# Kernel optimization log

Hardware: AMD Instinct MI355X
Metric: run time of the kernel (lower is better)

Reference implementation:

```python
import jax, jax.numpy as jnp
import numpy as np

WS = 15  # window_size


def setup_inputs() -> dict:
    key = jax.random.key(0)
    k1, k2, k3, k4 = jax.random.split(key, 4)
    x = jax.random.normal(k1, (4, 256, 200, 200), dtype=jnp.float32)
    theta_w = jax.random.normal(k2, (144, 256), dtype=jnp.float32) * 0.01
    phi_w = jax.random.normal(k3, (144, 256), dtype=jnp.float32) * 0.01
    # zero_init=False: use a small random projection so the output is nontrivial
    proj_w = jax.random.normal(k4, (256, 256), dtype=jnp.float32) * 0.01
    return {"x": x, "theta_w": theta_w, "phi_w": phi_w, "proj_w": proj_w}


def reference(x, theta_w, phi_w, proj_w):
    B, C, H, W = x.shape
    ws = WS
    pad_h = (ws - H % ws) % ws
    pad_w = (ws - W % ws) % ws
    xp = jnp.pad(x, ((0, 0), (0, 0), (0, pad_h), (0, pad_w)), mode='reflect')
    Hp, Wp = xp.shape[2], xp.shape[3]
    Nh, Nw = Hp // ws, Wp // ws
    # extract non-overlapping ws x ws windows -> (B*Nh*Nw, C, ws*ws)
    xw = (xp.reshape(B, C, Nh, ws, Nw, ws)
            .transpose(0, 2, 4, 1, 3, 5)
            .reshape(B * Nh * Nw, C, ws * ws))
    Ce = theta_w.shape[0]  # 144
    theta = jnp.einsum('ec,bcn->bne', theta_w, xw)   # (Bp, N, Ce)
    phi = jnp.einsum('ec,bcm->bem', phi_w, xw)       # (Bp, Ce, N)
    aff = jnp.einsum('bne,bem->bnm', theta, phi) / jnp.sqrt(jnp.asarray(Ce, x.dtype))
    aff = jax.nn.softmax(aff, axis=-1)               # (Bp, N, N)
    out = jnp.einsum('bnm,bcm->bcn', aff, xw)        # attention-weighted g (= x windows)
    out = jnp.einsum('oc,bcn->bon', proj_w, out)     # 1x1 projection
    # fold windows back -> (B, C, Hp, Wp), crop, residual
    y = (out.reshape(B, Nh, Nw, C, ws, ws)
            .transpose(0, 3, 1, 4, 2, 5)
            .reshape(B, C, Hp, Wp))
    y = y[:, :, :H, :W]
    return x + y
```

## Files before the change

kernel.cpp:

```cpp
#include <hip/hip_runtime.h>


#define WS_   15
#define B_    4
#define C_    256
#define H_    200
#define H2    (H_*H_)
#define NHW   14
#define NWIN  (B_*NHW*NHW)
#define NPOS  225
#define NWAVE 16

#define PT_STRIDE 144
#define Z_STRIDE  232
#define TT_STRIDE 144
#define ST_STRIDE 240
#define TT_SLOT   (16*TT_STRIDE)
#define ST_SLOT   (16*ST_STRIDE)

#define XT_OFF    0
#define PT_OFF    57600
#define Z_OFF     90144
#define TT_OFF    149536
#define ST_OFF    154144
#define GS_OFF    161824
#define LDS_BYTES 162016

typedef __attribute__((ext_vector_type(4))) float floatx4;

__device__ inline int pack4(float a, float b, float c, float d) {
    int pk = __builtin_amdgcn_cvt_pk_fp8_f32(a, b, 0, false);
    return __builtin_amdgcn_cvt_pk_fp8_f32(c, d, pk, true);
}
__device__ inline long wfrag8(const float* p, float scale) {
    floatx4 a = *(const floatx4*)p;
    floatx4 b = *(const floatx4*)(p + 4);
    int lo = 0, hi = 0;
    lo = __builtin_amdgcn_cvt_pk_fp8_f32(a[0]*scale, a[1]*scale, lo, false);
    lo = __builtin_amdgcn_cvt_pk_fp8_f32(a[2]*scale, a[3]*scale, lo, true);
    hi = __builtin_amdgcn_cvt_pk_fp8_f32(b[0]*scale, b[1]*scale, hi, false);
    hi = __builtin_amdgcn_cvt_pk_fp8_f32(b[2]*scale, b[3]*scale, hi, true);
    return ((long)(unsigned)lo) | (((long)(unsigned)hi) << 32);
}
__device__ inline long ldsfrag(const char* p) { return *(const long*)p; }

#define MFMA8(a,b,c) __builtin_amdgcn_mfma_f32_16x16x32_fp8_fp8((a),(b),(c),0,0,0)

__device__ inline void bar_lds() {
    asm volatile("s_waitcnt lgkmcnt(0)" ::: "memory");
    __builtin_amdgcn_s_barrier();
}

__global__ __launch_bounds__(1024) void wnl_kernel(
    const float* __restrict__ x, const float* __restrict__ theta_w,
    const float* __restrict__ phi_w, const float* __restrict__ proj_w,
    float* __restrict__ out)
{
    __shared__ char lds[LDS_BYTES];
    char*  XT    = lds + XT_OFF;
    char*  PT    = lds + PT_OFF;
    char*  Zs    = lds + Z_OFF;
    char*  TT    = lds + TT_OFF;
    char*  ST    = lds + ST_OFF;
    float* gsumf = (float*)(lds + GS_OFF);

    const int tid  = threadIdx.x;
    const int wv   = tid >> 6;
    const int lane = tid & 63;
    const int q    = lane >> 4;
    const int l16  = lane & 15;
    const int swl  = (l16 & 7) << 3;

    const int wid  = blockIdx.x;
    const int b    = wid / (NHW*NHW);
    const int rr   = wid % (NHW*NHW);
    const int row0 = (rr / NHW) * WS_;
    const int col0 = (rr % NHW) * WS_;
    const float* xb = x + (size_t)b * C_ * H2;

    long thw[8], wA[8], wB[8];
    if (wv < 9) {
        const float* wrow = theta_w + (wv*16 + l16) * C_ + q*8;
        #pragma unroll
        for (int ck = 0; ck < 8; ++ck) thw[ck] = wfrag8(wrow + ck*32, 16.f);
    }
    {
        const float* wrowA = (wv < 9)
            ? (phi_w  + (wv*16     + l16) * C_ + q*8)
            : (proj_w + ((wv-9)*16 + l16) * C_ + q*8);
        #pragma unroll
        for (int ck = 0; ck < 8; ++ck) wA[ck] = wfrag8(wrowA + ck*32, 16.f);
        if (wv < 9) {
            const float* wrowB = proj_w + ((wv+7)*16 + l16) * C_ + q*8;
            #pragma unroll
            for (int ck = 0; ck < 8; ++ck) wB[ck] = wfrag8(wrowB + ck*32, 16.f);
        }
    }

    if (tid < 48) gsumf[tid] = 0.f;

    {
        const int gn  = tid & 255;
        const int gc0 = (tid >> 8) << 2;
        if (gn < NPOS) {
            int wr = row0 + gn / WS_;
            int wc = col0 + gn % WS_;
            int gr = (wr < H_) ? wr : (2*H_ - 2 - wr);
            int gc = (wc < H_) ? wc : (2*H_ - 2 - wc);
            const float* p = xb + (size_t)gc0 * H2 + (gr * H_ + gc);
            char* dst = XT + gn * 256;
            const int sw = (gn & 7) << 3;
            float a0 = p[0], a1 = p[H2], a2 = p[2*(size_t)H2], a3 = p[3*(size_t)H2];
            for (int k = 0; k < 16; ++k) {
                float b0=0.f, b1=0.f, b2=0.f, b3=0.f;
                if (k < 15) {
                    const float* pn = p + (size_t)(16*(k+1)) * H2;
                    b0 = pn[0]; b1 = pn[H2]; b2 = pn[2*(size_t)H2]; b3 = pn[3*(size_t)H2];
                }
                *(int*)(dst + ((gc0 + 16*k) ^ sw)) = pack4(a0, a1, a2, a3);
                a0=b0; a1=b1; a2=b2; a3=b3;
            }
        }
    }
    bar_lds();

    if (wv < 9) {
        for (int mt = 0; mt < 15; ++mt) {
            long xf[8];
            const char* xbase = XT + (mt*16 + l16) * 256;
            #pragma unroll
            for (int ck = 0; ck < 8; ++ck)
                xf[ck] = ldsfrag(xbase + ((q*8 + ck*32) ^ swl));
            floatx4 accP = {0.f,0.f,0.f,0.f};
            floatx4 accZ = {0.f,0.f,0.f,0.f};
            #pragma unroll
            for (int ck = 0; ck < 8; ++ck) {
                accP = MFMA8(wA[ck], xf[ck], accP);
                accZ = MFMA8(xf[ck], wB[ck], accZ);
            }
            if (mt*16 + l16 < NPOS)
                *(int*)(PT + (mt*16 + l16) * PT_STRIDE + wv*16 + 4*q) =
                    pack4(accP[0], accP[1], accP[2], accP[3]);
            {
                float z[4];
                #pragma unroll
                for (int r = 0; r < 4; ++r) {
                    int m = mt*16 + 4*q + r;
                    z[r] = (m < NPOS) ? accZ[r] : 0.f;
                }
                if (mt*16 + 4*q < Z_STRIDE)
                    *(int*)(Zs + ((wv+7)*16 + l16) * Z_STRIDE + mt*16 + 4*q) =
                        pack4(z[0], z[1], z[2], z[3]);
            }
            if (mt == 0) {
                floatx4 accT = {0.f,0.f,0.f,0.f};
                #pragma unroll
                for (int ck = 0; ck < 8; ++ck)
                    accT = MFMA8(thw[ck], xf[ck], accT);
                *(int*)(TT + l16 * TT_STRIDE + wv*16 + 4*q) =
                    pack4(accT[0], accT[1], accT[2], accT[3]);
            }
        }
    } else {
        const int ot = wv - 9;
        for (int mt = 0; mt < 15; ++mt) {
            long xf[8];
            const char* xbase = XT + (mt*16 + l16) * 256;
            #pragma unroll
            for (int ck = 0; ck < 8; ++ck)
                xf[ck] = ldsfrag(xbase + ((q*8 + ck*32) ^ swl));
            floatx4 accZ = {0.f,0.f,0.f,0.f};
            #pragma unroll
            for (int ck = 0; ck < 8; ++ck)
                accZ = MFMA8(xf[ck], wA[ck], accZ);
            float z[4];
            #pragma unroll
            for (int r = 0; r < 4; ++r) {
                int m = mt*16 + 4*q + r;
                z[r] = (m < NPOS) ? accZ[r] : 0.f;
            }
            if (mt*16 + 4*q < Z_STRIDE)
                *(int*)(Zs + (ot*16 + l16) * Z_STRIDE + mt*16 + 4*q) =
                    pack4(z[0], z[1], z[2], z[3]);
        }
    }
    bar_lds();

    long pfr[5];
    if (wv < 15) {
        const char* prow = PT + (wv*16 + l16) * PT_STRIDE + q*8;
        #pragma unroll
        for (int kk = 0; kk < 4; ++kk) pfr[kk] = ldsfrag(prow + kk*32);
        pfr[4] = (q < 2) ? ldsfrag(PT + (wv*16 + l16)*PT_STRIDE + 128 + q*8) : 0L;
    }
    long zfr[8];
    {
        const char* zrow = Zs + (wv*16 + l16) * Z_STRIDE + q*8;
        #pragma unroll
        for (int km = 0; km < 7; ++km) zfr[km] = ldsfrag(zrow + km*32);
        zfr[7] = (q == 0) ? ldsfrag(Zs + (wv*16 + l16)*Z_STRIDE + 224) : 0L;
    }

    for (int nt = 0; nt <= 15; ++nt) {
        const bool do_aff = (nt < 15) && (wv < 15);
        const bool do_pv  = (nt >= 1);
        const bool do_tt  = (nt < 14) && (wv < 9);

        float xr0=0.f, xr1=0.f, xr2=0.f, xr3=0.f;
        size_t gbase = 0; bool valid = false;
        if (do_pv) {
            const int n_o  = (nt-1)*16 + l16;
            const int wr_o = row0 + n_o / WS_;
            const int wc_o = col0 + n_o % WS_;
            valid = (n_o < NPOS) && (wr_o < H_) && (wc_o < H_);
            gbase = (((size_t)b * C_ + (wv*16 + q*4)) * H_ + wr_o) * H_ + wc_o;
            if (valid) {
                xr0 = x[gbase];
                xr1 = x[gbase + H2];
                xr2 = x[gbase + 2*(size_t)H2];
                xr3 = x[gbase + 3*(size_t)H2];
            }
        }

        floatx4 aacc = {0.f,0.f,0.f,0.f};
        if (do_aff) {
            const char* trow = TT + (nt & 1) * TT_SLOT + l16 * TT_STRIDE + q*8;
            long tfr[5];
            #pragma unroll
            for (int kk = 0; kk < 4; ++kk) tfr[kk] = ldsfrag(trow + kk*32);
            tfr[4] = (q < 2)
                ? ldsfrag(TT + (nt & 1) * TT_SLOT + l16 * TT_STRIDE + 128 + q*8) : 0L;
            #pragma unroll
            for (int kk = 0; kk < 4; ++kk)
                aacc = MFMA8(pfr[kk], tfr[kk], aacc);
            aacc = MFMA8(pfr[4], tfr[4], aacc);
        }
        float pe[4] = {0.f,0.f,0.f,0.f};
        if (do_aff) {
            #pragma unroll
            for (int r = 0; r < 4; ++r) {
                int m = wv*16 + 4*q + r;
                pe[r] = (m < NPOS) ? __expf(aacc[r] * (1.0f/3072.0f)) : 0.f;
            }
        }

        long sfr[8];
        if (do_pv) {
            const char* srow = ST + ((nt-1) & 1) * ST_SLOT + l16 * ST_STRIDE + q*8;
            #pragma unroll
            for (int km = 0; km < 7; ++km) sfr[km] = ldsfrag(srow + km*32);
            sfr[7] = (q == 0)
                ? ldsfrag(ST + ((nt-1) & 1) * ST_SLOT + l16 * ST_STRIDE + 224) : 0L;
        }
        long xf[8];
        if (do_tt) {
            const char* xbase = XT + ((nt+1)*16 + l16) * 256;
            #pragma unroll
            for (int ck = 0; ck < 8; ++ck)
                xf[ck] = ldsfrag(xbase + ((q*8 + ck*32) ^ swl));
        }

        if (do_aff) {
            *(int*)(ST + (nt & 1) * ST_SLOT + l16 * ST_STRIDE + wv*16 + 4*q) =
                pack4(pe[0], pe[1], pe[2], pe[3]);
            float s = pe[0] + pe[1] + pe[2] + pe[3];
            s += __shfl_xor(s, 16);
            s += __shfl_xor(s, 32);
            if (lane < 16) atomicAdd(&gsumf[(nt % 3)*16 + lane], s);
        }
        if (do_tt) {
            floatx4 tacc = {0.f,0.f,0.f,0.f};
            #pragma unroll
            for (int ck = 0; ck < 8; ++ck)
                tacc = MFMA8(thw[ck], xf[ck], tacc);
            *(int*)(TT + ((nt+1) & 1) * TT_SLOT + l16 * TT_STRIDE + wv*16 + 4*q) =
                pack4(tacc[0], tacc[1], tacc[2], tacc[3]);
        }
        if (do_pv) {
            floatx4 acc = {0.f,0.f,0.f,0.f};
            #pragma unroll
            for (int km = 0; km < 7; ++km)
                acc = MFMA8(zfr[km], sfr[km], acc);
            acc = MFMA8(zfr[7], sfr[7], acc);
            float gs   = gsumf[((nt-1) % 3)*16 + l16];
            float sinv = __builtin_amdgcn_rcpf(16.0f * gs);
            if (valid) {
                __builtin_nontemporal_store(xr0 + acc[0]*sinv, &out[gbase]);
                __builtin_nontemporal_store(xr1 + acc[1]*sinv, &out[gbase + H2]);
                __builtin_nontemporal_store(xr2 + acc[2]*sinv, &out[gbase + 2*(size_t)H2]);
                __builtin_nontemporal_store(xr3 + acc[3]*sinv, &out[gbase + 3*(size_t)H2]);
            }
        }
        if (wv == 15 && lane < 16 && nt < 15)
            gsumf[((nt+1) % 3)*16 + lane] = 0.f;

        if (nt < 15) bar_lds();
    }
}

extern "C" void kernel_launch(void* const* d_in, const int* in_sizes, int n_in,
                              void* d_out, int out_size, void* d_ws, size_t ws_size,
                              hipStream_t stream) {
    (void)in_sizes; (void)n_in; (void)out_size; (void)d_ws; (void)ws_size;
    const float* x   = (const float*)d_in[0];
    const float* tw  = (const float*)d_in[1];
    const float* pw  = (const float*)d_in[2];
    const float* prw = (const float*)d_in[3];
    wnl_kernel<<<NWIN, 1024, 0, stream>>>(x, tw, pw, prw, (float*)d_out);
}
```

Before: 623.2 us.

## Restructure window kernel so each wave owns one query tile end-to-end

```diff
diff --git a/kernel.cpp b/kernel.cpp
--- a/kernel.cpp
+++ b/kernel.cpp
@@ -11,20 +11,19 @@
 #define NPOS  225
 #define NWAVE 16
 
+#define XT_STRIDE 264
 #define PT_STRIDE 144
-#define Z_STRIDE  232
-#define TT_STRIDE 144
-#define ST_STRIDE 240
-#define TT_SLOT   (16*TT_STRIDE)
-#define ST_SLOT   (16*ST_STRIDE)
-
-#define XT_OFF    0
-#define PT_OFF    57600
-#define Z_OFF     90144
-#define TT_OFF    149536
-#define ST_OFF    154144
-#define GS_OFF    161824
-#define LDS_BYTES 162016
+#define Z_STRIDE  240
+
+#define XT_OFF 0
+#define PT_OFF 59400
+#define Z_OFF  91800
+#define LDS_BYTES 153240
+
+#define THQ_OFF 0
+#define PHQ_OFF 36864
+#define PRQ_OFF 73728
+#define WQ_BYTES 139264
 
 typedef __attribute__((ext_vector_type(4))) float floatx4;
 
@@ -32,17 +31,8 @@
     int pk = __builtin_amdgcn_cvt_pk_fp8_f32(a, b, 0, false);
     return __builtin_amdgcn_cvt_pk_fp8_f32(c, d, pk, true);
 }
-__device__ inline long wfrag8(const float* p, float scale) {
-    floatx4 a = *(const floatx4*)p;
-    floatx4 b = *(const floatx4*)(p + 4);
-    int lo = 0, hi = 0;
-    lo = __builtin_amdgcn_cvt_pk_fp8_f32(a[0]*scale, a[1]*scale, lo, false);
-    lo = __builtin_amdgcn_cvt_pk_fp8_f32(a[2]*scale, a[3]*scale, lo, true);
-    hi = __builtin_amdgcn_cvt_pk_fp8_f32(b[0]*scale, b[1]*scale, hi, false);
-    hi = __builtin_amdgcn_cvt_pk_fp8_f32(b[2]*scale, b[3]*scale, hi, true);
-    return ((long)(unsigned)lo) | (((long)(unsigned)hi) << 32);
-}
 __device__ inline long ldsfrag(const char* p) { return *(const long*)p; }
+__device__ inline long gfrag(const unsigned char* p) { return *(const long*)p; }
 
 #define MFMA8(a,b,c) __builtin_amdgcn_mfma_f32_16x16x32_fp8_fp8((a),(b),(c),0,0,0)
 
@@ -51,25 +41,38 @@
     __builtin_amdgcn_s_barrier();
 }
 
+__global__ void prep_kernel(const float* __restrict__ tw,
+                            const float* __restrict__ pw,
+                            const float* __restrict__ prw,
+                            unsigned char* __restrict__ wq)
+{
+    int idx = blockIdx.x * blockDim.x + threadIdx.x;
+    for (int d = idx; d < WQ_BYTES / 4; d += gridDim.x * blockDim.x) {
+        int base = d * 4;
+        const float* src;
+        int off;
+        if (base < PHQ_OFF)      { src = tw;  off = base; }
+        else if (base < PRQ_OFF) { src = pw;  off = base - PHQ_OFF; }
+        else                     { src = prw; off = base - PRQ_OFF; }
+        const float* p = src + off;
+        ((int*)wq)[d] = pack4(p[0]*16.f, p[1]*16.f, p[2]*16.f, p[3]*16.f);
+    }
+}
+
 __global__ __launch_bounds__(1024) void wnl_kernel(
-    const float* __restrict__ x, const float* __restrict__ theta_w,
-    const float* __restrict__ phi_w, const float* __restrict__ proj_w,
+    const float* __restrict__ x, const unsigned char* __restrict__ wq,
     float* __restrict__ out)
 {
     __shared__ char lds[LDS_BYTES];
-    char*  XT    = lds + XT_OFF;
-    char*  PT    = lds + PT_OFF;
-    char*  Zs    = lds + Z_OFF;
-    char*  TT    = lds + TT_OFF;
-    char*  ST    = lds + ST_OFF;
-    float* gsumf = (float*)(lds + GS_OFF);
+    char* XT = lds + XT_OFF;
+    char* PT = lds + PT_OFF;
+    char* Zs = lds + Z_OFF;
 
     const int tid  = threadIdx.x;
     const int wv   = tid >> 6;
     const int lane = tid & 63;
     const int q    = lane >> 4;
     const int l16  = lane & 15;
-    const int swl  = (l16 & 7) << 3;
 
     const int wid  = blockIdx.x;
     const int b    = wid / (NHW*NHW);
@@ -78,26 +81,21 @@
     const int col0 = (rr % NHW) * WS_;
     const float* xb = x + (size_t)b * C_ * H2;
 
-    long thw[8], wA[8], wB[8];
+    const unsigned char* thetaq = wq + THQ_OFF;
+    const unsigned char* phiq   = wq + PHQ_OFF;
+    const unsigned char* projq  = wq + PRQ_OFF;
+
+    long wAf[8], wBf[8];
     if (wv < 9) {
-        const float* wrow = theta_w + (wv*16 + l16) * C_ + q*8;
-        #pragma unroll
-        for (int ck = 0; ck < 8; ++ck) thw[ck] = wfrag8(wrow + ck*32, 16.f);
-    }
-    {
-        const float* wrowA = (wv < 9)
-            ? (phi_w  + (wv*16     + l16) * C_ + q*8)
-            : (proj_w + ((wv-9)*16 + l16) * C_ + q*8);
-        #pragma unroll
-        for (int ck = 0; ck < 8; ++ck) wA[ck] = wfrag8(wrowA + ck*32, 16.f);
-        if (wv < 9) {
-            const float* wrowB = proj_w + ((wv+7)*16 + l16) * C_ + q*8;
-            #pragma unroll
-            for (int ck = 0; ck < 8; ++ck) wB[ck] = wfrag8(wrowB + ck*32, 16.f);
-        }
-    }
-
-    if (tid < 48) gsumf[tid] = 0.f;
+        const unsigned char* pa = phiq + (wv*16 + l16)*256 + q*8;
+        const unsigned char* pb = projq + ((wv+7)*16 + l16)*256 + q*8;
+        #pragma unroll
+        for (int ck = 0; ck < 8; ++ck) { wAf[ck] = gfrag(pa + ck*32); wBf[ck] = gfrag(pb + ck*32); }
+    } else {
+        const unsigned char* pa = projq + ((wv-9)*16 + l16)*256 + q*8;
+        #pragma unroll
+        for (int ck = 0; ck < 8; ++ck) wAf[ck] = gfrag(pa + ck*32);
+    }
 
     {
         const int gn  = tid & 255;
@@ -108,8 +106,7 @@
             int gr = (wr < H_) ? wr : (2*H_ - 2 - wr);
             int gc = (wc < H_) ? wc : (2*H_ - 2 - wc);
             const float* p = xb + (size_t)gc0 * H2 + (gr * H_ + gc);
-            char* dst = XT + gn * 256;
-            const int sw = (gn & 7) << 3;
+            char* dst = XT + gn * XT_STRIDE;
             float a0 = p[0], a1 = p[H2], a2 = p[2*(size_t)H2], a3 = p[3*(size_t)H2];
             for (int k = 0; k < 16; ++k) {
                 float b0=0.f, b1=0.f, b2=0.f, b3=0.f;
@@ -117,7 +114,7 @@
                     const float* pn = p + (size_t)(16*(k+1)) * H2;
                     b0 = pn[0]; b1 = pn[H2]; b2 = pn[2*(size_t)H2]; b3 = pn[3*(size_t)H2];
                 }
-                *(int*)(dst + ((gc0 + 16*k) ^ sw)) = pack4(a0, a1, a2, a3);
+                *(int*)(dst + gc0 + 16*k) = pack4(a0, a1, a2, a3);
                 a0=b0; a1=b1; a2=b2; a3=b3;
             }
         }
@@ -127,184 +124,179 @@
     if (wv < 9) {
         for (int mt = 0; mt < 15; ++mt) {
             long xf[8];
-            const char* xbase = XT + (mt*16 + l16) * 256;
-            #pragma unroll
-            for (int ck = 0; ck < 8; ++ck)
-                xf[ck] = ldsfrag(xbase + ((q*8 + ck*32) ^ swl));
+            const char* xrow = XT + (mt*16 + l16) * XT_STRIDE + q*8;
+            #pragma unroll
+            for (int ck = 0; ck < 8; ++ck) xf[ck] = ldsfrag(xrow + ck*32);
             floatx4 accP = {0.f,0.f,0.f,0.f};
             floatx4 accZ = {0.f,0.f,0.f,0.f};
             #pragma unroll
             for (int ck = 0; ck < 8; ++ck) {
-                accP = MFMA8(wA[ck], xf[ck], accP);
-                accZ = MFMA8(xf[ck], wB[ck], accZ);
+                accP = MFMA8(wAf[ck], xf[ck], accP);
+                accZ = MFMA8(xf[ck], wBf[ck], accZ);
             }
             if (mt*16 + l16 < NPOS)
                 *(int*)(PT + (mt*16 + l16) * PT_STRIDE + wv*16 + 4*q) =
                     pack4(accP[0], accP[1], accP[2], accP[3]);
-            {
-                float z[4];
-                #pragma unroll
-                for (int r = 0; r < 4; ++r) {
-                    int m = mt*16 + 4*q + r;
-                    z[r] = (m < NPOS) ? accZ[r] : 0.f;
-                }
-                if (mt*16 + 4*q < Z_STRIDE)
-                    *(int*)(Zs + ((wv+7)*16 + l16) * Z_STRIDE + mt*16 + 4*q) =
-                        pack4(z[0], z[1], z[2], z[3]);
-            }
-            if (mt == 0) {
-                floatx4 accT = {0.f,0.f,0.f,0.f};
-                #pragma unroll
-                for (int ck = 0; ck < 8; ++ck)
-                    accT = MFMA8(thw[ck], xf[ck], accT);
-                *(int*)(TT + l16 * TT_STRIDE + wv*16 + 4*q) =
-                    pack4(accT[0], accT[1], accT[2], accT[3]);
-            }
+            float z[4];
+            #pragma unroll
+            for (int r = 0; r < 4; ++r) {
+                int m = mt*16 + 4*q + r;
+                z[r] = (m < NPOS) ? accZ[r] : 0.f;
+            }
+            *(int*)(Zs + ((wv+7)*16 + l16) * Z_STRIDE + mt*16 + 4*q) =
+                pack4(z[0], z[1], z[2], z[3]);
         }
     } else {
         const int ot = wv - 9;
         for (int mt = 0; mt < 15; ++mt) {
             long xf[8];
-            const char* xbase = XT + (mt*16 + l16) * 256;
+            const char* xrow = XT + (mt*16 + l16) * XT_STRIDE + q*8;
+            #pragma unroll
+            for (int ck = 0; ck < 8; ++ck) xf[ck] = ldsfrag(xrow + ck*32);
+            floatx4 accZ = {0.f,0.f,0.f,0.f};
             #pragma unroll
             for (int ck = 0; ck < 8; ++ck)
-                xf[ck] = ldsfrag(xbase + ((q*8 + ck*32) ^ swl));
-            floatx4 accZ = {0.f,0.f,0.f,0.f};
-            #pragma unroll
-            for (int ck = 0; ck < 8; ++ck)
-                accZ = MFMA8(xf[ck], wA[ck], accZ);
+                accZ = MFMA8(xf[ck], wAf[ck], accZ);
             float z[4];
             #pragma unroll
             for (int r = 0; r < 4; ++r) {
                 int m = mt*16 + 4*q + r;
                 z[r] = (m < NPOS) ? accZ[r] : 0.f;
             }
-            if (mt*16 + 4*q < Z_STRIDE)
-                *(int*)(Zs + (ot*16 + l16) * Z_STRIDE + mt*16 + 4*q) =
-                    pack4(z[0], z[1], z[2], z[3]);
+            *(int*)(Zs + (ot*16 + l16) * Z_STRIDE + mt*16 + 4*q) =
+                pack4(z[0], z[1], z[2], z[3]);
         }
     }
     bar_lds();
 
-    long pfr[5];
     if (wv < 15) {
-        const char* prow = PT + (wv*16 + l16) * PT_STRIDE + q*8;
-        #pragma unroll
-        for (int kk = 0; kk < 4; ++kk) pfr[kk] = ldsfrag(prow + kk*32);
-        pfr[4] = (q < 2) ? ldsfrag(PT + (wv*16 + l16)*PT_STRIDE + 128 + q*8) : 0L;
-    }
-    long zfr[8];
-    {
-        const char* zrow = Zs + (wv*16 + l16) * Z_STRIDE + q*8;
-        #pragma unroll
-        for (int km = 0; km < 7; ++km) zfr[km] = ldsfrag(zrow + km*32);
-        zfr[7] = (q == 0) ? ldsfrag(Zs + (wv*16 + l16)*Z_STRIDE + 224) : 0L;
-    }
-
-    for (int nt = 0; nt <= 15; ++nt) {
-        const bool do_aff = (nt < 15) && (wv < 15);
-        const bool do_pv  = (nt >= 1);
-        const bool do_tt  = (nt < 14) && (wv < 9);
-
+        const int nt = wv;
+        const int srcA = l16 + ((q & 1) << 5);
+        const int srcB = srcA + 16;
+
+        long xf[8];
+        {
+            const char* xrow = XT + (nt*16 + l16) * XT_STRIDE + q*8;
+            #pragma unroll
+            for (int ck = 0; ck < 8; ++ck) xf[ck] = ldsfrag(xrow + ck*32);
+        }
+
+        int pkT[9];
+        #pragma unroll
+        for (int et = 0; et < 9; ++et) {
+            const unsigned char* tp = thetaq + (et*16 + l16)*256 + q*8;
+            long tf[8];
+            #pragma unroll
+            for (int ck = 0; ck < 8; ++ck) tf[ck] = gfrag(tp + ck*32);
+            floatx4 acc = {0.f,0.f,0.f,0.f};
+            #pragma unroll
+            for (int ck = 0; ck < 8; ++ck)
+                acc = MFMA8(tf[ck], xf[ck], acc);
+            pkT[et] = pack4(acc[0], acc[1], acc[2], acc[3]);
+        }
+        long tfr[5];
+        #pragma unroll
+        for (int kk = 0; kk < 4; ++kk) {
+            int a0 = __shfl(pkT[2*kk],   srcA);
+            int a1 = __shfl(pkT[2*kk+1], srcA);
+            int b0 = __shfl(pkT[2*kk],   srcB);
+            int b1 = __shfl(pkT[2*kk+1], srcB);
+            unsigned lo = (q >= 2) ? (unsigned)a1 : (unsigned)a0;
+            unsigned hi = (q >= 2) ? (unsigned)b1 : (unsigned)b0;
+            tfr[kk] = (long)lo | ((long)hi << 32);
+        }
+        {
+            int a8 = __shfl(pkT[8], srcA);
+            int b8 = __shfl(pkT[8], srcB);
+            tfr[4] = (q < 2) ? ((long)(unsigned)a8 | ((long)(unsigned)b8 << 32)) : 0L;
+        }
+
+        float ssum = 0.f;
+        int pm[15];
+        #pragma unroll
+        for (int mt = 0; mt < 15; ++mt) {
+            const char* prow = PT + (mt*16 + l16) * PT_STRIDE + q*8;
+            floatx4 aacc = {0.f,0.f,0.f,0.f};
+            #pragma unroll
+            for (int kk = 0; kk < 4; ++kk)
+                aacc = MFMA8(ldsfrag(prow + kk*32), tfr[kk], aacc);
+            long p4 = (q < 2) ? ldsfrag(PT + (mt*16 + l16)*PT_STRIDE + 128 + q*8) : 0L;
+            aacc = MFMA8(p4, tfr[4], aacc);
+            float pe[4];
+            #pragma unroll
+            for (int r = 0; r < 4; ++r) {
+                int m = mt*16 + 4*q + r;
+                pe[r] = (m < NPOS) ? __expf(aacc[r] * (1.0f/3072.0f)) : 0.f;
+                ssum += pe[r];
+            }
+            pm[mt] = pack4(pe[0], pe[1], pe[2], pe[3]);
+        }
+        ssum += __shfl_xor(ssum, 16);
+        ssum += __shfl_xor(ssum, 32);
+        const float sinv = __builtin_amdgcn_rcpf(16.0f * ssum);
+
+        long sfr[8];
+        #pragma unroll
+        for (int km = 0; km < 7; ++km) {
+            int a0 = __shfl(pm[2*km],   srcA);
+            int a1 = __shfl(pm[2*km+1], srcA);
+            int b0 = __shfl(pm[2*km],   srcB);
+            int b1 = __shfl(pm[2*km+1], srcB);
+            unsigned lo = (q >= 2) ? (unsigned)a1 : (unsigned)a0;
+            unsigned hi = (q >= 2) ? (unsigned)b1 : (unsigned)b0;
+            sfr[km] = (long)lo | ((long)hi << 32);
+        }
+        {
+            int a8 = __shfl(pm[14], srcA);
+            int b8 = __shfl(pm[14], srcB);
+            sfr[7] = (q == 0) ? ((long)(unsigned)a8 | ((long)(unsigned)b8 << 32)) : 0L;
+        }
+
+        const int n_o  = nt*16 + l16;
+        const int wr_o = row0 + n_o / WS_;
+        const int wc_o = col0 + n_o % WS_;
+        const bool valid = (n_o < NPOS) && (wr_o < H_) && (wc_o < H_);
+        const size_t gb0 = (size_t)b * C_ * H2 + ((size_t)wr_o * H_ + wc_o);
         float xr0=0.f, xr1=0.f, xr2=0.f, xr3=0.f;
-        size_t gbase = 0; bool valid = false;
-        if (do_pv) {
-            const int n_o  = (nt-1)*16 + l16;
-            const int wr_o = row0 + n_o / WS_;
-            const int wc_o = col0 + n_o % WS_;
-            valid = (n_o < NPOS) && (wr_o < H_) && (wc_o < H_);
-            gbase = (((size_t)b * C_ + (wv*16 + q*4)) * H_ + wr_o) * H_ + wc_o;
+        if (valid) {
+            const float* p = x + gb0 + (size_t)(4*q) * H2;
+            xr0 = p[0]; xr1 = p[H2]; xr2 = p[2*(size_t)H2]; xr3 = p[3*(size_t)H2];
+        }
+        #pragma unroll
+        for (int ot = 0; ot < 16; ++ot) {
+            float nx0=0.f, nx1=0.f, nx2=0.f, nx3=0.f;
+            if (ot < 15 && valid) {
+                const float* p = x + gb0 + (size_t)((ot+1)*16 + 4*q) * H2;
+                nx0 = p[0]; nx1 = p[H2]; nx2 = p[2*(size_t)H2]; nx3 = p[3*(size_t)H2];
+            }
+            const char* zrow = Zs + (ot*16 + l16) * Z_STRIDE + q*8;
+            floatx4 acc = {0.f,0.f,0.f,0.f};
+            #pragma unroll
+            for (int km = 0; km < 7; ++km)
+                acc = MFMA8(ldsfrag(zrow + km*32), sfr[km], acc);
+            long z7 = (q < 2) ? ldsfrag(Zs + (ot*16 + l16)*Z_STRIDE + 224 + q*8) : 0L;
+            acc = MFMA8(z7, sfr[7], acc);
             if (valid) {
-                xr0 = x[gbase];
-                xr1 = x[gbase + H2];
-                xr2 = x[gbase + 2*(size_t)H2];
-                xr3 = x[gbase + 3*(size_t)H2];
-            }
-        }
-
-        floatx4 aacc = {0.f,0.f,0.f,0.f};
-        if (do_aff) {
-            const char* trow = TT + (nt & 1) * TT_SLOT + l16 * TT_STRIDE + q*8;
-            long tfr[5];
-            #pragma unroll
-            for (int kk = 0; kk < 4; ++kk) tfr[kk] = ldsfrag(trow + kk*32);
-            tfr[4] = (q < 2)
-                ? ldsfrag(TT + (nt & 1) * TT_SLOT + l16 * TT_STRIDE + 128 + q*8) : 0L;
-            #pragma unroll
-            for (int kk = 0; kk < 4; ++kk)
-                aacc = MFMA8(pfr[kk], tfr[kk], aacc);
-            aacc = MFMA8(pfr[4], tfr[4], aacc);
-        }
-        float pe[4] = {0.f,0.f,0.f,0.f};
-        if (do_aff) {
-            #pragma unroll
-            for (int r = 0; r < 4; ++r) {
-                int m = wv*16 + 4*q + r;
-                pe[r] = (m < NPOS) ? __expf(aacc[r] * (1.0f/3072.0f)) : 0.f;
-            }
-        }
-
-        long sfr[8];
-        if (do_pv) {
-            const char* srow = ST + ((nt-1) & 1) * ST_SLOT + l16 * ST_STRIDE + q*8;
-            #pragma unroll
-            for (int km = 0; km < 7; ++km) sfr[km] = ldsfrag(srow + km*32);
-            sfr[7] = (q == 0)
-                ? ldsfrag(ST + ((nt-1) & 1) * ST_SLOT + l16 * ST_STRIDE + 224) : 0L;
-        }
-        long xf[8];
-        if (do_tt) {
-            const char* xbase = XT + ((nt+1)*16 + l16) * 256;
-            #pragma unroll
-            for (int ck = 0; ck < 8; ++ck)
-                xf[ck] = ldsfrag(xbase + ((q*8 + ck*32) ^ swl));
-        }
-
-        if (do_aff) {
-            *(int*)(ST + (nt & 1) * ST_SLOT + l16 * ST_STRIDE + wv*16 + 4*q) =
-                pack4(pe[0], pe[1], pe[2], pe[3]);
-            float s = pe[0] + pe[1] + pe[2] + pe[3];
-            s += __shfl_xor(s, 16);
-            s += __shfl_xor(s, 32);
-            if (lane < 16) atomicAdd(&gsumf[(nt % 3)*16 + lane], s);
-        }
-        if (do_tt) {
-            floatx4 tacc = {0.f,0.f,0.f,0.f};
-            #pragma unroll
-            for (int ck = 0; ck < 8; ++ck)
-                tacc = MFMA8(thw[ck], xf[ck], tacc);
-            *(int*)(TT + ((nt+1) & 1) * TT_SLOT + l16 * TT_STRIDE + wv*16 + 4*q) =
-                pack4(tacc[0], tacc[1], tacc[2], tacc[3]);
-        }
-        if (do_pv) {
-            floatx4 acc = {0.f,0.f,0.f,0.f};
-            #pragma unroll
-            for (int km = 0; km < 7; ++km)
-                acc = MFMA8(zfr[km], sfr[km], acc);
-            acc = MFMA8(zfr[7], sfr[7], acc);
-            float gs   = gsumf[((nt-1) % 3)*16 + l16];
-            float sinv = __builtin_amdgcn_rcpf(16.0f * gs);
-            if (valid) {
-                __builtin_nontemporal_store(xr0 + acc[0]*sinv, &out[gbase]);
-                __builtin_nontemporal_store(xr1 + acc[1]*sinv, &out[gbase + H2]);
-                __builtin_nontemporal_store(xr2 + acc[2]*sinv, &out[gbase + 2*(size_t)H2]);
-                __builtin_nontemporal_store(xr3 + acc[3]*sinv, &out[gbase + 3*(size_t)H2]);
-            }
-        }
-        if (wv == 15 && lane < 16 && nt < 15)
-            gsumf[((nt+1) % 3)*16 + lane] = 0.f;
-
-        if (nt < 15) bar_lds();
+                float* o0 = out + gb0 + (size_t)(ot*16 + 4*q) * H2;
+                __builtin_nontemporal_store(xr0 + acc[0]*sinv, o0);
+                __builtin_nontemporal_store(xr1 + acc[1]*sinv, o0 + H2);
+                __builtin_nontemporal_store(xr2 + acc[2]*sinv, o0 + 2*(size_t)H2);
+                __builtin_nontemporal_store(xr3 + acc[3]*sinv, o0 + 3*(size_t)H2);
+            }
+            xr0=nx0; xr1=nx1; xr2=nx2; xr3=nx3;
+        }
     }
 }
 
 extern "C" void kernel_launch(void* const* d_in, const int* in_sizes, int n_in,
                               void* d_out, int out_size, void* d_ws, size_t ws_size,
                               hipStream_t stream) {
-    (void)in_sizes; (void)n_in; (void)out_size; (void)d_ws; (void)ws_size;
+    (void)in_sizes; (void)n_in; (void)out_size; (void)ws_size;
     const float* x   = (const float*)d_in[0];
     const float* tw  = (const float*)d_in[1];
     const float* pw  = (const float*)d_in[2];
     const float* prw = (const float*)d_in[3];
-    wnl_kernel<<<NWIN, 1024, 0, stream>>>(x, tw, pw, prw, (float*)d_out);
-}
+    unsigned char* wqd = (unsigned char*)d_ws;
+    prep_kernel<<<64, 256, 0, stream>>>(tw, pw, prw, wqd);
+    wnl_kernel<<<NWIN, 1024, 0, stream>>>(x, wqd, (float*)d_out);
+}
```

New measurement: 667.9 us. +7.2%, slower.
